# Performance work log

Hardware: AMD Instinct MI355X
Metric: run time of the kernel (lower is better)

The kernel has to match this reference:

```python
import jax, jax.numpy as jnp
import numpy as np

NUM_HEADS = 16


def setup_inputs() -> dict:
    key = jax.random.key(0)
    k1, k2, k3 = jax.random.split(key, 3)
    B, S, D = 4, 2048, 1024
    hidden_states = jax.random.normal(k1, (B, S, D), dtype=jnp.float32)
    w_qkv = jax.random.normal(k2, (D, 3 * D), dtype=jnp.float32) * (1.0 / np.sqrt(D))
    w_out = jax.random.normal(k3, (D, D), dtype=jnp.float32) * (1.0 / np.sqrt(D))
    return {"hidden_states": hidden_states, "w_qkv": w_qkv, "w_out": w_out}


def reference(hidden_states, w_qkv, w_out):
    B, S, D = hidden_states.shape
    H = NUM_HEADS
    d = D // H
    # fused QKV projection: [B, S, 3D] -> [3, B, S, H, d]
    qkv = (hidden_states @ w_qkv).reshape(B, S, 3, H, d)
    q, k, v = jnp.moveaxis(qkv, 2, 0)  # each [B, S, H, d]
    scale = 1.0 / np.sqrt(d).astype(np.float32)
    scores = jnp.einsum("bqhd,bkhd->bhqk", q, k) * scale  # [B, H, S, S]
    attn = jax.nn.softmax(scores, axis=-1)
    ctx = jnp.einsum("bhqk,bkhd->bqhd", attn, v).reshape(B, S, D)
    return ctx @ w_out
```

## Files before the change

### kernel.cpp

```cpp
#include <hip/hip_runtime.h>
#include <hip/hip_bf16.h>
#include <math.h>

typedef __bf16 bf16;
typedef __bf16 bf16x4 __attribute__((ext_vector_type(4)));
typedef __bf16 bf16x8 __attribute__((ext_vector_type(8)));
typedef float  f32x4  __attribute__((ext_vector_type(4)));

#define B_  4
#define S_  2048
#define D_  1024
#define H_  16
#define DH  64
#define M_  (B_*S_)
#define BH_ (B_*H_)

#define QSCALE 0.18033688011112042f

__device__ __forceinline__ void glds16(const bf16* g, bf16* l) {
  __builtin_amdgcn_global_load_lds((const __attribute__((address_space(1))) void*)g,
                                   (__attribute__((address_space(3))) void*)l, 16, 0, 0);
}

__global__ void cvt_f32_bf16(const float* __restrict__ in, bf16* __restrict__ out, int n) {
  int i = (blockIdx.x * 256 + threadIdx.x) * 4;
  if (i < n) {
    float4 v = *(const float4*)(in + i);
    bf16x4 o = { (bf16)v.x, (bf16)v.y, (bf16)v.z, (bf16)v.w };
    *(bf16x4*)(out + i) = o;
  }
}

__global__ void transpose_cvt2(const float* __restrict__ wqkv, const float* __restrict__ wout,
                               bf16* __restrict__ wqkvT, bf16* __restrict__ woutT) {
  __shared__ float tile[32][33];
  int bx = blockIdx.x;
  const float* in; bf16* out; int C, c0;
  if (bx < 96) { in = wqkv; out = wqkvT; C = 3072; c0 = bx * 32; }
  else         { in = wout; out = woutT; C = 1024; c0 = (bx - 96) * 32; }
  int tx = threadIdx.x, ty = threadIdx.y;
  int r0 = blockIdx.y * 32;
  #pragma unroll
  for (int i = ty; i < 32; i += 8) tile[i][tx] = in[(size_t)(r0 + i) * C + c0 + tx];
  __syncthreads();
  #pragma unroll
  for (int i = ty; i < 32; i += 8) out[(size_t)(c0 + i) * D_ + r0 + tx] = (bf16)tile[tx][i];
}

#define LDA2 32

__device__ __forceinline__ void gemm_core(const bf16* __restrict__ A, const bf16* __restrict__ Bt,
                                          int m0, int n0, bf16* As, bf16* Bs,
                                          int tid, f32x4 acc[4][4]) {
  int wave = tid >> 6, lane = tid & 63, quad = lane >> 4, l16 = lane & 15;
  int wm = (wave >> 1) * 64, wn = (wave & 1) * 64;
  int lr = lane >> 2, lc = (lane & 3) * 8;
  const bf16* gA = A  + (size_t)(m0 + wave * 32 + lr) * D_ + lc;
  const bf16* gB = Bt + (size_t)(n0 + wave * 32 + lr) * D_ + lc;
  bf16* lA = As + wave * 32 * LDA2;
  bf16* lB = Bs + wave * 32 * LDA2;
  for (int k0 = 0; k0 < D_; k0 += 32) {
    glds16(gA + k0,           lA);
    glds16(gA + k0 + 16 * D_, lA + 16 * LDA2);
    glds16(gB + k0,           lB);
    glds16(gB + k0 + 16 * D_, lB + 16 * LDA2);
    __syncthreads();
    bf16x8 af[4], bff[4];
    #pragma unroll
    for (int i = 0; i < 4; i++) af[i]  = *(const bf16x8*)(As + (wm + i * 16 + l16) * LDA2 + quad * 8);
    #pragma unroll
    for (int j = 0; j < 4; j++) bff[j] = *(const bf16x8*)(Bs + (wn + j * 16 + l16) * LDA2 + quad * 8);
    #pragma unroll
    for (int i = 0; i < 4; i++)
      #pragma unroll
      for (int j = 0; j < 4; j++)
        acc[i][j] = __builtin_amdgcn_mfma_f32_16x16x32_bf16(af[i], bff[j], acc[i][j], 0, 0, 0);
    __syncthreads();
  }
}

__global__ __launch_bounds__(256) void gemm_qkv(const bf16* __restrict__ A, const bf16* __restrict__ Bt,
                                                bf16* __restrict__ Qb, bf16* __restrict__ Kb,
                                                bf16* __restrict__ Vtb) {
  __shared__ __attribute__((aligned(16))) bf16 As[128 * LDA2];
  __shared__ __attribute__((aligned(16))) bf16 Bs[128 * LDA2];
  int tid = threadIdx.x;
  int m0 = blockIdx.y * 128, n0 = blockIdx.x * 128;
  f32x4 acc[4][4] = {};
  gemm_core(A, Bt, m0, n0, As, Bs, tid, acc);
  int wave = tid >> 6, lane = tid & 63, quad = lane >> 4, l16 = lane & 15;
  int wm = (wave >> 1) * 64, wn = (wave & 1) * 64;
  int which = n0 >> 10;
  if (which == 2) {
    #pragma unroll
    for (int i = 0; i < 4; i++) {
      int mb = m0 + wm + i * 16 + quad * 4;
      int b = mb >> 11, s = mb & 2047;
      #pragma unroll
      for (int j = 0; j < 4; j++) {
        int n = n0 + wn + j * 16 + l16;
        int h = (n >> 6) & 15, dd = n & 63;
        bf16x4 v4 = { (bf16)acc[i][j][0], (bf16)acc[i][j][1], (bf16)acc[i][j][2], (bf16)acc[i][j][3] };
        *(bf16x4*)(Vtb + ((size_t)(b * H_ + h) * DH + dd) * S_ + s) = v4;
      }
    }
  } else {
    bf16* dst = (which == 0) ? Qb : Kb;
    float sc = (which == 0) ? QSCALE : 1.0f;
    #pragma unroll
    for (int i = 0; i < 4; i++) {
      #pragma unroll
      for (int j = 0; j < 4; j++) {
        int n = n0 + wn + j * 16 + l16;
        int h = (n >> 6) & 15, dd = n & 63;
        #pragma unroll
        for (int r = 0; r < 4; r++) {
          int m = m0 + wm + i * 16 + quad * 4 + r;
          int b = m >> 11, s = m & 2047;
          dst[(((size_t)(b * H_ + h)) * S_ + s) * DH + dd] = (bf16)(acc[i][j][r] * sc);
        }
      }
    }
  }
}

__global__ __launch_bounds__(256) void gemm_out(const bf16* __restrict__ A, const bf16* __restrict__ Bt,
                                                float* __restrict__ C) {
  __shared__ __attribute__((aligned(16))) bf16 As[128 * LDA2];
  __shared__ __attribute__((aligned(16))) bf16 Bs[128 * LDA2];
  int tid = threadIdx.x;
  int m0 = blockIdx.y * 128, n0 = blockIdx.x * 128;
  f32x4 acc[4][4] = {};
  gemm_core(A, Bt, m0, n0, As, Bs, tid, acc);
  int wave = tid >> 6, lane = tid & 63, quad = lane >> 4, l16 = lane & 15;
  int wm = (wave >> 1) * 64, wn = (wave & 1) * 64;
  #pragma unroll
  for (int i = 0; i < 4; i++)
    #pragma unroll
    for (int j = 0; j < 4; j++) {
      int n = n0 + wn + j * 16 + l16;
      #pragma unroll
      for (int r = 0; r < 4; r++) {
        int m = m0 + wm + i * 16 + quad * 4 + r;
        C[(size_t)m * D_ + n] = acc[i][j][r];
      }
    }
}

#define LDK 72
#define LDP 40
#define NT  (S_ / 64)

__global__ __launch_bounds__(256, 2) void attn(const bf16* __restrict__ Qb, const bf16* __restrict__ Kb,
                                               const bf16* __restrict__ Vtb, bf16* __restrict__ ctx) {
  __shared__ __attribute__((aligned(16))) bf16 Ks[2][64 * LDK];
  __shared__ __attribute__((aligned(16))) bf16 Vs[2][64 * LDK];
  __shared__ __attribute__((aligned(16))) bf16 Ps[4][64 * LDP];
  int tid = threadIdx.x;
  int wave = tid >> 6, lane = tid & 63, quad = lane >> 4, l16 = lane & 15;
  int bh = blockIdx.x;
  int b = bh >> 4, h = bh & 15;
  int q0 = blockIdx.y * 256 + wave * 64;
  const bf16* Qp = Qb  + (size_t)bh * S_ * DH;
  const bf16* Kp = Kb  + (size_t)bh * S_ * DH;
  const bf16* Vp = Vtb + (size_t)bh * DH * S_;

  int srow = tid >> 3, scc = (tid & 7) << 3;

  bf16x8 qf[4][2];
  #pragma unroll
  for (int nq = 0; nq < 4; nq++)
    #pragma unroll
    for (int ks = 0; ks < 2; ks++)
      qf[nq][ks] = *(const bf16x8*)(Qp + (size_t)(q0 + nq * 16 + l16) * DH + ks * 32 + quad * 8);

  bf16 one1 = (bf16)1.0f;
  bf16x8 onesf = { one1, one1, one1, one1, one1, one1, one1, one1 };

  f32x4 o[4][4] = {};
  f32x4 oden[4] = {};

  {
    bf16x8 k0a = *(const bf16x8*)(Kp + (size_t)srow * DH + scc);
    bf16x8 k0b = *(const bf16x8*)(Kp + (size_t)(32 + srow) * DH + scc);
    bf16x8 v0a = *(const bf16x8*)(Vp + (size_t)srow * S_ + scc);
    bf16x8 v0b = *(const bf16x8*)(Vp + (size_t)(32 + srow) * S_ + scc);
    *(bf16x8*)(Ks[0] + srow * LDK + scc)        = k0a;
    *(bf16x8*)(Ks[0] + (32 + srow) * LDK + scc) = k0b;
    *(bf16x8*)(Vs[0] + srow * LDK + scc)        = v0a;
    *(bf16x8*)(Vs[0] + (32 + srow) * LDK + scc) = v0b;
  }

  for (int kt = 0; kt < NT; kt++) {
    int cur = kt & 1;
    __syncthreads();

    bf16x8 ka, kb2, va, vb;
    if (kt + 1 < NT) {
      const bf16* Kn = Kp + (size_t)(kt + 1) * 64 * DH;
      const bf16* Vn = Vp + (size_t)(kt + 1) * 64;
      ka  = *(const bf16x8*)(Kn + (size_t)srow * DH + scc);
      kb2 = *(const bf16x8*)(Kn + (size_t)(32 + srow) * DH + scc);
      va  = *(const bf16x8*)(Vn + (size_t)srow * S_ + scc);
      vb  = *(const bf16x8*)(Vn + (size_t)(32 + srow) * S_ + scc);
    }

    bf16x8 vf[4][2];
    #pragma unroll
    for (int td = 0; td < 4; td++)
      #pragma unroll
      for (int ks = 0; ks < 2; ks++)
        vf[td][ks] = *(const bf16x8*)(Vs[cur] + (td * 16 + l16) * LDK + ks * 32 + quad * 8);

    #pragma unroll
    for (int hh = 0; hh < 2; hh++) {
      #pragma unroll
      for (int kq2 = 0; kq2 < 2; kq2++) {
        int kq = hh * 2 + kq2;
        bf16x8 kfr[2];
        #pragma unroll
        for (int ks = 0; ks < 2; ks++)
          kfr[ks] = *(const bf16x8*)(Ks[cur] + (kq * 16 + l16) * LDK + ks * 32 + quad * 8);
        #pragma unroll
        for (int nq = 0; nq < 4; nq++) {
          f32x4 st = {};
          st = __builtin_amdgcn_mfma_f32_16x16x32_bf16(kfr[0], qf[nq][0], st, 0, 0, 0);
          st = __builtin_amdgcn_mfma_f32_16x16x32_bf16(kfr[1], qf[nq][1], st, 0, 0, 0);
          bf16x4 pk;
          #pragma unroll
          for (int r = 0; r < 4; r++) pk[r] = (bf16)__builtin_amdgcn_exp2f(st[r]);
          *(bf16x4*)(&Ps[wave][(nq * 16 + l16) * LDP + kq2 * 16 + quad * 4]) = pk;
        }
      }
      #pragma unroll
      for (int nq = 0; nq < 4; nq++) {
        bf16x8 pf = *(const bf16x8*)(&Ps[wave][(nq * 16 + l16) * LDP + quad * 8]);
        oden[nq] = __builtin_amdgcn_mfma_f32_16x16x32_bf16(pf, onesf, oden[nq], 0, 0, 0);
        #pragma unroll
        for (int td = 0; td < 4; td++)
          o[nq][td] = __builtin_amdgcn_mfma_f32_16x16x32_bf16(pf, vf[td][hh], o[nq][td], 0, 0, 0);
      }
    }

    if (kt + 1 < NT) {
      int nxt = cur ^ 1;
      *(bf16x8*)(Ks[nxt] + srow * LDK + scc)        = ka;
      *(bf16x8*)(Ks[nxt] + (32 + srow) * LDK + scc) = kb2;
      *(bf16x8*)(Vs[nxt] + srow * LDK + scc)        = va;
      *(bf16x8*)(Vs[nxt] + (32 + srow) * LDK + scc) = vb;
    }
  }

  #pragma unroll
  for (int nq = 0; nq < 4; nq++) {
    #pragma unroll
    for (int r = 0; r < 4; r++) {
      float inv = 1.0f / oden[nq][r];
      int q = q0 + nq * 16 + quad * 4 + r;
      #pragma unroll
      for (int td = 0; td < 4; td++) {
        int dd = td * 16 + l16;
        ctx[((size_t)(b * S_) + q) * D_ + h * DH + dd] = (bf16)(o[nq][td][r] * inv);
      }
    }
  }
}

extern "C" void kernel_launch(void* const* d_in, const int* in_sizes, int n_in,
                              void* d_out, int out_size, void* d_ws, size_t ws_size,
                              hipStream_t stream) {
  (void)in_sizes; (void)n_in; (void)out_size; (void)ws_size;
  const float* hidden = (const float*)d_in[0];
  const float* w_qkv  = (const float*)d_in[1];
  const float* w_out  = (const float*)d_in[2];
  float* out = (float*)d_out;

  char* ws = (char*)d_ws;
  size_t off = 0;
  bf16* hb    = (bf16*)(ws + off); off += (size_t)M_ * D_ * 2;
  bf16* wqkvT = (bf16*)(ws + off); off += (size_t)3 * D_ * D_ * 2;
  bf16* woutT = (bf16*)(ws + off); off += (size_t)D_ * D_ * 2;
  bf16* Qb    = (bf16*)(ws + off); off += (size_t)M_ * D_ * 2;
  bf16* Kb    = (bf16*)(ws + off); off += (size_t)M_ * D_ * 2;
  bf16* Vtb   = (bf16*)(ws + off); off += (size_t)M_ * D_ * 2;
  bf16* ctxb  = hb;

  cvt_f32_bf16<<<(M_ * D_ / 4 + 255) / 256, 256, 0, stream>>>(hidden, hb, M_ * D_);
  transpose_cvt2<<<dim3(128, D_ / 32), dim3(32, 8), 0, stream>>>(w_qkv, w_out, wqkvT, woutT);
  gemm_qkv<<<dim3(3 * D_ / 128, M_ / 128), 256, 0, stream>>>(hb, wqkvT, Qb, Kb, Vtb);
  attn<<<dim3(BH_, S_ / 256), 256, 0, stream>>>(Qb, Kb, Vtb, ctxb);
  gemm_out<<<dim3(D_ / 128, M_ / 128), 256, 0, stream>>>(ctxb, woutT, out);
}
```

Baseline: 266.3 us.

## Merge prep kernels, double GEMM k-step per barrier, reorder out-GEMM grid

Combines the hidden-state conversion and the weight transpose/convert into one prep launch, which saves one kernel launch. The GEMM core now loads two 32-wide k-slices into twice the LDS before each barrier pair, so the loop needs half as many barriers at the cost of larger shared memory per block. The output GEMM grid swaps its x and y mapping so that consecutive blocks walk along M, which changes how the weight and activation tiles are reused in cache.

```diff
diff --git a/kernel.cpp b/kernel.cpp
--- a/kernel.cpp
+++ b/kernel.cpp
@@ -22,24 +22,23 @@
                                    (__attribute__((address_space(3))) void*)l, 16, 0, 0);
 }
 
-__global__ void cvt_f32_bf16(const float* __restrict__ in, bf16* __restrict__ out, int n) {
-  int i = (blockIdx.x * 256 + threadIdx.x) * 4;
-  if (i < n) {
-    float4 v = *(const float4*)(in + i);
+__global__ __launch_bounds__(256) void prep(const float* __restrict__ hidden, bf16* __restrict__ hb,
+                                            const float* __restrict__ wqkv, const float* __restrict__ wout,
+                                            bf16* __restrict__ wqkvT, bf16* __restrict__ woutT) {
+  int bx = blockIdx.x, tid = threadIdx.x;
+  if (bx < 8192) {
+    int i = (bx * 256 + tid) * 4;
+    float4 v = *(const float4*)(hidden + i);
     bf16x4 o = { (bf16)v.x, (bf16)v.y, (bf16)v.z, (bf16)v.w };
-    *(bf16x4*)(out + i) = o;
-  }
-}
-
-__global__ void transpose_cvt2(const float* __restrict__ wqkv, const float* __restrict__ wout,
-                               bf16* __restrict__ wqkvT, bf16* __restrict__ woutT) {
+    *(bf16x4*)(hb + i) = o;
+    return;
+  }
   __shared__ float tile[32][33];
-  int bx = blockIdx.x;
-  const float* in; bf16* out; int C, c0;
-  if (bx < 96) { in = wqkv; out = wqkvT; C = 3072; c0 = bx * 32; }
-  else         { in = wout; out = woutT; C = 1024; c0 = (bx - 96) * 32; }
-  int tx = threadIdx.x, ty = threadIdx.y;
-  int r0 = blockIdx.y * 32;
+  int t = bx - 8192;
+  const float* in; bf16* out; int C, c0, r0;
+  if (t < 96 * 32) { in = wqkv; out = wqkvT; C = 3072; c0 = (t % 96) * 32; r0 = (t / 96) * 32; }
+  else { t -= 96 * 32;  in = wout; out = woutT; C = 1024; c0 = (t % 32) * 32; r0 = (t / 32) * 32; }
+  int tx = tid & 31, ty = tid >> 5;
   #pragma unroll
   for (int i = ty; i < 32; i += 8) tile[i][tx] = in[(size_t)(r0 + i) * C + c0 + tx];
   __syncthreads();
@@ -48,6 +47,7 @@
 }
 
 #define LDA2 32
+#define SUB  (128 * LDA2)
 
 __device__ __forceinline__ void gemm_core(const bf16* __restrict__ A, const bf16* __restrict__ Bt,
                                           int m0, int n0, bf16* As, bf16* Bs,
@@ -59,22 +59,29 @@
   const bf16* gB = Bt + (size_t)(n0 + wave * 32 + lr) * D_ + lc;
   bf16* lA = As + wave * 32 * LDA2;
   bf16* lB = Bs + wave * 32 * LDA2;
-  for (int k0 = 0; k0 < D_; k0 += 32) {
-    glds16(gA + k0,           lA);
-    glds16(gA + k0 + 16 * D_, lA + 16 * LDA2);
-    glds16(gB + k0,           lB);
-    glds16(gB + k0 + 16 * D_, lB + 16 * LDA2);
+  for (int k0 = 0; k0 < D_; k0 += 64) {
+    #pragma unroll
+    for (int h = 0; h < 2; h++) {
+      int kk = k0 + h * 32;
+      glds16(gA + kk,           lA + h * SUB);
+      glds16(gA + kk + 16 * D_, lA + h * SUB + 16 * LDA2);
+      glds16(gB + kk,           lB + h * SUB);
+      glds16(gB + kk + 16 * D_, lB + h * SUB + 16 * LDA2);
+    }
     __syncthreads();
-    bf16x8 af[4], bff[4];
-    #pragma unroll
-    for (int i = 0; i < 4; i++) af[i]  = *(const bf16x8*)(As + (wm + i * 16 + l16) * LDA2 + quad * 8);
-    #pragma unroll
-    for (int j = 0; j < 4; j++) bff[j] = *(const bf16x8*)(Bs + (wn + j * 16 + l16) * LDA2 + quad * 8);
-    #pragma unroll
-    for (int i = 0; i < 4; i++)
-      #pragma unroll
-      for (int j = 0; j < 4; j++)
-        acc[i][j] = __builtin_amdgcn_mfma_f32_16x16x32_bf16(af[i], bff[j], acc[i][j], 0, 0, 0);
+    #pragma unroll
+    for (int h = 0; h < 2; h++) {
+      bf16x8 af[4], bff[4];
+      #pragma unroll
+      for (int i = 0; i < 4; i++) af[i]  = *(const bf16x8*)(As + h * SUB + (wm + i * 16 + l16) * LDA2 + quad * 8);
+      #pragma unroll
+      for (int j = 0; j < 4; j++) bff[j] = *(const bf16x8*)(Bs + h * SUB + (wn + j * 16 + l16) * LDA2 + quad * 8);
+      #pragma unroll
+      for (int i = 0; i < 4; i++)
+        #pragma unroll
+        for (int j = 0; j < 4; j++)
+          acc[i][j] = __builtin_amdgcn_mfma_f32_16x16x32_bf16(af[i], bff[j], acc[i][j], 0, 0, 0);
+    }
     __syncthreads();
   }
 }
@@ -82,8 +89,8 @@
 __global__ __launch_bounds__(256) void gemm_qkv(const bf16* __restrict__ A, const bf16* __restrict__ Bt,
                                                 bf16* __restrict__ Qb, bf16* __restrict__ Kb,
                                                 bf16* __restrict__ Vtb) {
-  __shared__ __attribute__((aligned(16))) bf16 As[128 * LDA2];
-  __shared__ __attribute__((aligned(16))) bf16 Bs[128 * LDA2];
+  __shared__ __attribute__((aligned(16))) bf16 As[2 * SUB];
+  __shared__ __attribute__((aligned(16))) bf16 Bs[2 * SUB];
   int tid = threadIdx.x;
   int m0 = blockIdx.y * 128, n0 = blockIdx.x * 128;
   f32x4 acc[4][4] = {};
@@ -126,10 +133,10 @@
 
 __global__ __launch_bounds__(256) void gemm_out(const bf16* __restrict__ A, const bf16* __restrict__ Bt,
                                                 float* __restrict__ C) {
-  __shared__ __attribute__((aligned(16))) bf16 As[128 * LDA2];
-  __shared__ __attribute__((aligned(16))) bf16 Bs[128 * LDA2];
+  __shared__ __attribute__((aligned(16))) bf16 As[2 * SUB];
+  __shared__ __attribute__((aligned(16))) bf16 Bs[2 * SUB];
   int tid = threadIdx.x;
-  int m0 = blockIdx.y * 128, n0 = blockIdx.x * 128;
+  int m0 = blockIdx.x * 128, n0 = blockIdx.y * 128;
   f32x4 acc[4][4] = {};
   gemm_core(A, Bt, m0, n0, As, Bs, tid, acc);
   int wave = tid >> 6, lane = tid & 63, quad = lane >> 4, l16 = lane & 15;
@@ -285,9 +292,8 @@
   bf16* Vtb   = (bf16*)(ws + off); off += (size_t)M_ * D_ * 2;
   bf16* ctxb  = hb;
 
-  cvt_f32_bf16<<<(M_ * D_ / 4 + 255) / 256, 256, 0, stream>>>(hidden, hb, M_ * D_);
-  transpose_cvt2<<<dim3(128, D_ / 32), dim3(32, 8), 0, stream>>>(w_qkv, w_out, wqkvT, woutT);
+  prep<<<8192 + 96 * 32 + 32 * 32, 256, 0, stream>>>(hidden, hb, w_qkv, w_out, wqkvT, woutT);
   gemm_qkv<<<dim3(3 * D_ / 128, M_ / 128), 256, 0, stream>>>(hb, wqkvT, Qb, Kb, Vtb);
   attn<<<dim3(BH_, S_ / 256), 256, 0, stream>>>(Qb, Kb, Vtb, ctxb);
-  gemm_out<<<dim3(D_ / 128, M_ / 128), 256, 0, stream>>>(ctxb, woutT, out);
-}
+  gemm_out<<<dim3(M_ / 128, D_ / 128), 256, 0, stream>>>(ctxb, woutT, out);
+}
```

After: 251.4 us. 1.06x faster.
